# Optimization experiments

Hardware: AMD Instinct MI355X
Metric: run time of the kernel (lower is better)

Reference implementation:

```python
import jax, jax.numpy as jnp
import numpy as np
from jax import lax

H = 128  # hidden_size
E = 4    # embed_size
L = 4    # num_layers


def gru_cell(x, h, wih, whh, bih, bhh):
    # x: [B, in], h: [B, H]; PyTorch gate order: r, z, n
    gi = x @ wih.T + bih          # [B, 3H]
    gh = h @ whh.T + bhh          # [B, 3H]
    ir, iz, inn = jnp.split(gi, 3, axis=-1)
    hr, hz, hn = jnp.split(gh, 3, axis=-1)
    r = jax.nn.sigmoid(ir + hr)
    z = jax.nn.sigmoid(iz + hz)
    n = jnp.tanh(inn + r * hn)
    return (1.0 - z) * n + z * h


def multilayer_gru_step(hidden, x_t, wih0, whh0, wih, whh, bih, bhh):
    # hidden: [L, B, H], x_t: [B, E] -> (new_hidden [L,B,H], top_out [B,H])
    hs = []
    h0 = gru_cell(x_t, hidden[0], wih0, whh0, bih[0], bhh[0])
    hs.append(h0)
    inp = h0
    for l in range(1, L):
        hl = gru_cell(inp, hidden[l], wih[l - 1], whh[l - 1], bih[l], bhh[l])
        hs.append(hl)
        inp = hl
    return jnp.stack(hs, axis=0), inp


def setup_inputs() -> dict:
    key = jax.random.key(0)
    ks = jax.random.split(key, 20)
    s = 1.0 / np.sqrt(H)
    u = lambda k, shp: jax.random.uniform(k, shp, jnp.float32, -s, s)
    inp = {
        'inp_tensor': jax.random.normal(ks[0], (4096, 64, E), jnp.float32),
        'tgt_tensor': jax.random.normal(ks[1], (4096, 100, E), jnp.float32),
        # encoder GRU params
        'enc_wih0': u(ks[2], (3 * H, E)),
        'enc_whh0': u(ks[3], (3 * H, H)),
        'enc_wih': u(ks[4], (L - 1, 3 * H, H)),
        'enc_whh': u(ks[5], (L - 1, 3 * H, H)),
        'enc_bih': u(ks[6], (L, 3 * H)),
        'enc_bhh': u(ks[7], (L, 3 * H)),
        # decoder GRU params
        'dec_wih0': u(ks[8], (3 * H, E)),
        'dec_whh0': u(ks[9], (3 * H, H)),
        'dec_wih': u(ks[10], (L - 1, 3 * H, H)),
        'dec_whh': u(ks[11], (L - 1, 3 * H, H)),
        'dec_bih': u(ks[12], (L, 3 * H)),
        'dec_bhh': u(ks[13], (L, 3 * H)),
        # decoder MLP params
        'lin1_w': u(ks[14], (H, H)),
        'lin1_b': u(ks[15], (H,)),
        'lin2_w': u(ks[16], (E, H)),
        'lin2_b': u(ks[17], (E,)),
    }
    return inp


def reference(inp_tensor, tgt_tensor, enc_wih0, enc_whh0, enc_wih, enc_whh,
              enc_bih, enc_bhh, dec_wih0, dec_whh0, dec_wih, dec_whh,
              dec_bih, dec_bhh, lin1_w, lin1_b, lin2_w, lin2_b):
    B = inp_tensor.shape[0]
    T = tgt_tensor.shape[1]

    # ---- encoder: scan over source time ----
    h_init = jnp.zeros((L, B, H), inp_tensor.dtype)

    def enc_step(hidden, x_t):
        new_h, top = multilayer_gru_step(hidden, x_t, enc_wih0, enc_whh0,
                                         enc_wih, enc_whh, enc_bih, enc_bhh)
        return new_h, top

    enc_hidden, enc_outs = lax.scan(enc_step, h_init,
                                    jnp.transpose(inp_tensor, (1, 0, 2)))
    encoder_output = jnp.transpose(enc_outs, (1, 0, 2))  # [B, S, H]

    # ---- decoder: teacher forcing, target_length-1 steps ----
    # decoder inputs: [inp[:,0], tgt[:,1], ..., tgt[:,T-2]]; tgt part detached
    dec_inputs = jnp.concatenate(
        [inp_tensor[:, 0:1, :], lax.stop_gradient(tgt_tensor[:, 1:T - 1, :])], axis=1)
    dec_targets = tgt_tensor[:, 1:T, :]  # [B, T-1, E]

    def dec_step(hidden, xy):
        x_t, y_t = xy
        new_h, top = multilayer_gru_step(hidden, x_t, dec_wih0, dec_whh0,
                                         dec_wih, dec_whh, dec_bih, dec_bhh)
        o = jax.nn.relu(top @ lin1_w.T + lin1_b) @ lin2_w.T + lin2_b  # [B, E]
        step_loss = jnp.mean((o - y_t) ** 2)
        return new_h, (o, step_loss)

    dec_hidden, (dec_outs, step_losses) = lax.scan(
        dec_step, enc_hidden,
        (jnp.transpose(dec_inputs, (1, 0, 2)), jnp.transpose(dec_targets, (1, 0, 2))))
    loss = jnp.sum(step_losses)
    decoder_output = jnp.concatenate(
        [inp_tensor[:, 0:1, :], jnp.transpose(dec_outs, (1, 0, 2))], axis=1)  # [B, T, E]

    return decoder_output, dec_hidden, encoder_output, enc_hidden, loss
```

## Files before the change

kernel.cpp:

```cpp
#include <hip/hip_runtime.h>

#define T_ENC 64
#define T_DEC 99

#define SLOT    16384
#define PH_BLOB 393216
#define O_LIN1  786432
#define W_TOTAL 802816

#define DEC_OUT_OFF 0
#define DEC_HID_OFF 1638400
#define ENC_OUT_OFF 3735552
#define ENC_HID_OFF 37289984
#define LOSS_OFF    39387136

typedef float f32x4 __attribute__((ext_vector_type(4)));
typedef int   v8i  __attribute__((ext_vector_type(8)));
typedef long  v4l  __attribute__((ext_vector_type(4)));

__device__ __forceinline__ v8i as8i(v4l x) {
  union { v4l l; v8i i; } u; u.l = x; return u.i;
}

__device__ __forceinline__ void keep(v4l &x) { asm volatile("" : "+v"(x)); }
__device__ __forceinline__ void keep(long &x) { asm volatile("" : "+v"(x)); }

#define MFMA8(a, b, c) __builtin_amdgcn_mfma_f32_16x16x32_fp8_fp8((a), (b), (c), 0, 0, 0)
#define MFMAS(a, b, c) \
  __builtin_amdgcn_mfma_scale_f32_16x16x128_f8f6f4(as8i(a), as8i(b), (c), 0, 0, 0, 127, 0, 127)

__device__ __forceinline__ unsigned f2fp8pk(float a, float b) {
  return (unsigned)__builtin_amdgcn_cvt_pk_fp8_f32(a, b, 0, false);
}
__device__ __forceinline__ float sigm(float x) {
  return __builtin_amdgcn_rcpf(1.f + __expf(-x));
}
__device__ __forceinline__ float tanh_fast(float x) {
  x = fminf(fmaxf(x, -15.f), 15.f);
  float e = __expf(-2.f * x);
  return (1.f - e) * __builtin_amdgcn_rcpf(1.f + e);
}

__global__ void convert_weights(const float* __restrict__ ewih0, const float* __restrict__ ewhh0,
                                const float* __restrict__ ewih, const float* __restrict__ ewhh,
                                const float* __restrict__ dwih0, const float* __restrict__ dwhh0,
                                const float* __restrict__ dwih, const float* __restrict__ dwhh,
                                const float* __restrict__ lin1w, unsigned char* __restrict__ wb) {
  int i = blockIdx.x * 256 + threadIdx.x;
  if (i >= W_TOTAL) return;
  float v;
  if (i < O_LIN1) {
    const int ph = i / PH_BLOB;
    const int li = i % PH_BLOB;
    const float* wih0 = ph ? dwih0 : ewih0;
    const float* whh0 = ph ? dwhh0 : ewhh0;
    const float* wih  = ph ? dwih  : ewih;
    const float* whh  = ph ? dwhh  : ewhh;
    const int l = li / (6 * SLOT);
    const int r6 = li % (6 * SLOT);
    const int s = r6 / SLOT, r = r6 % SLOT;
    const int g = (s < 3) ? s : (s - 3);
    if (s >= 3 && l == 0) {
      const int w = r >> 11, ks = (r >> 9) & 3, lane = (r >> 3) & 63, e = r & 7;
      const int quad = lane >> 4, ln = lane & 15;
      const int row = g * 128 + w * 16 + ln;
      const int col = ks * 32 + quad * 8 + e;
      v = (col < 4) ? wih0[row * 4 + col] : 0.f;
    } else {
      const int w = r >> 11, lane = (r >> 5) & 63, b = r & 31;
      const int quad = lane >> 4, ln = lane & 15;
      const int row = g * 128 + w * 16 + ln;
      const int col = quad * 32 + b;
      v = (s < 3) ? ((l == 0) ? whh0[row * 128 + col]
                              : whh[(l - 1) * 49152 + row * 128 + col])
                  : wih[(l - 1) * 49152 + row * 128 + col];
    }
  } else {
    const int r = i - O_LIN1;
    const int w = r >> 11, lane = (r >> 5) & 63, b = r & 31;
    const int quad = lane >> 4, ln = lane & 15;
    v = lin1w[(w * 16 + ln) * 128 + quad * 32 + b];
  }
  wb[i] = (unsigned char)(f2fp8pk(v, v) & 0xFF);
}

__global__ void zero_loss_k(float* out) { out[LOSS_OFF] = 0.f; }

__global__ __launch_bounds__(512, 2) void gru_seq2seq(
    const float* __restrict__ inp, const float* __restrict__ tgt,
    const float* __restrict__ enc_bih, const float* __restrict__ enc_bhh,
    const float* __restrict__ dec_bih, const float* __restrict__ dec_bhh,
    const float* __restrict__ lin1_b, const float* __restrict__ lin2_w,
    const float* __restrict__ lin2_b, const unsigned char* __restrict__ wb,
    float* __restrict__ out) {
  const int tid = threadIdx.x;
  const int wave = tid >> 6;
  const int lane = tid & 63;
  const int ln = lane & 15;
  const int quad = lane >> 4;
  const int b0 = blockIdx.x * 16;
  const int j = (wave << 4) + ln;

  __shared__ __align__(16) unsigned char hb8[2][4][16][128];
  __shared__ __align__(16) unsigned char xt8[2][16][128];
  __shared__ float bsum[4][2][128];
  __shared__ float bnn[4][2][128];
  __shared__ float lin1bs[128];
  __shared__ __align__(16) float lin2ws[4][132];
  __shared__ float lin2bs[4];
  __shared__ __align__(16) float relu_s[16][132];

  for (int i = tid; i < 2 * 4 * 16 * 128; i += 512) ((unsigned char*)hb8)[i] = 0;
  for (int i = tid; i < 2 * 16 * 128; i += 512) ((unsigned char*)xt8)[i] = 0;
  if (tid < 128) lin1bs[tid] = lin1_b[tid];
  { int e = tid >> 7, k = tid & 127; lin2ws[e][k] = lin2_w[e * 128 + k]; }
  if (tid < 4) lin2bs[tid] = lin2_b[tid];

  float hreg[4][4];
#pragma unroll
  for (int l = 0; l < 4; l++)
#pragma unroll
    for (int r = 0; r < 4; r++) hreg[l][r] = 0.f;

  float loss_local = 0.f;

  if (tid < 64) {
    int m = tid >> 2, e = tid & 3;
    out[DEC_OUT_OFF + (b0 + m) * 400 + e] = inp[(b0 + m) * 256 + e];
  }

  const int fofs32 = wave * 2048 + lane * 32;
  const int fofs8  = wave * 2048 + lane * 8;

  v4l w1v = *(const v4l*)(wb + O_LIN1 + fofs32);
  keep(w1v);

#pragma unroll 1
  for (int ph = 0; ph < 2; ph++) {
    const float* bih = ph ? dec_bih : enc_bih;
    const float* bhh = ph ? dec_bhh : enc_bhh;
    {
      int l = tid >> 7, jj = tid & 127;
      bsum[l][0][jj] = bih[l * 384 + jj] + bhh[l * 384 + jj];
      bsum[l][1][jj] = bih[l * 384 + 128 + jj] + bhh[l * 384 + 128 + jj];
      bnn[l][0][jj] = bih[l * 384 + 256 + jj];
      bnn[l][1][jj] = bhh[l * 384 + 256 + jj];
    }
    if (tid < 64) {
      int m = tid >> 2, e = tid & 3;
      xt8[0][m][(m << 3) | e] =
          (unsigned char)(f2fp8pk(inp[(b0 + m) * 256 + e], 0.f) & 0xFF);
    }
    __syncthreads();

    const unsigned char* PB = wb + ph * PH_BLOB;
    v4l whv[4][3];
    v4l wxv[3][3];
    long wx0f[3];
#pragma unroll
    for (int l = 0; l < 4; l++)
#pragma unroll
      for (int g = 0; g < 3; g++) {
        whv[l][g] = *(const v4l*)(PB + l * 6 * SLOT + g * SLOT + fofs32);
        keep(whv[l][g]);
      }
#pragma unroll
    for (int l = 1; l < 4; l++)
#pragma unroll
      for (int g = 0; g < 3; g++) {
        wxv[l - 1][g] = *(const v4l*)(PB + l * 6 * SLOT + (3 + g) * SLOT + fofs32);
        keep(wxv[l - 1][g]);
      }
#pragma unroll
    for (int g = 0; g < 3; g++) {
      wx0f[g] = *(const long*)(PB + (3 + g) * SLOT + fofs8);
      keep(wx0f[g]);
    }

    const float l1b = lin1bs[j];
    const int T = ph ? T_DEC : T_ENC;

#pragma unroll 1
    for (int t = 0; t < T; t++) {
      const int p = t & 1;
#pragma unroll
      for (int l = 0; l < 4; l++) {
        f32x4 ar = {0.f, 0.f, 0.f, 0.f}, az = {0.f, 0.f, 0.f, 0.f};
        f32x4 ani = {0.f, 0.f, 0.f, 0.f}, anh = {0.f, 0.f, 0.f, 0.f};
        {
          const unsigned char* ahb = &hb8[1 - p][l][0][0] + ln * 128;
          v4l Ah;
#pragma unroll
          for (int i4 = 0; i4 < 4; i4++)
            Ah[i4] = *(const long*)(ahb + ((((quad * 4 + i4) ^ ln) << 3)));
          ar  = MFMAS(Ah, whv[l][0], ar);
          az  = MFMAS(Ah, whv[l][1], az);
          anh = MFMAS(Ah, whv[l][2], anh);
        }
        if (l > 0) {
          const unsigned char* axb = &hb8[p][l - 1][0][0] + ln * 128;
          v4l Ax;
#pragma unroll
          for (int i4 = 0; i4 < 4; i4++)
            Ax[i4] = *(const long*)(axb + ((((quad * 4 + i4) ^ ln) << 3)));
          ar  = MFMAS(Ax, wxv[l - 1][0], ar);
          az  = MFMAS(Ax, wxv[l - 1][1], az);
          ani = MFMAS(Ax, wxv[l - 1][2], ani);
        } else {
          const unsigned char* axb = &xt8[p][0][0] + ln * 128;
          const long a_x0 = *(const long*)(axb + ((quad ^ ln) << 3));
          ar  = MFMA8(a_x0, wx0f[0], ar);
          az  = MFMA8(a_x0, wx0f[1], az);
          ani = MFMA8(a_x0, wx0f[2], ani);
        }
        const float brl = bsum[l][0][j], bzl = bsum[l][1][j];
        const float binl = bnn[l][0][j], bhnl = bnn[l][1][j];
        float hnv[4];
#pragma unroll
        for (int r = 0; r < 4; r++) {
          const int m = quad * 4 + r;
          const float hp = hreg[l][r];
          const float rg = sigm(ar[r] + brl);
          const float zg = sigm(az[r] + bzl);
          const float ng = tanh_fast(ani[r] + binl + rg * (anh[r] + bhnl));
          const float hn = (1.f - zg) * ng + zg * hp;
          hreg[l][r] = hn;
          hnv[r] = hn;
          if (!ph) {
            if (l == 3) out[ENC_OUT_OFF + ((b0 + m) * 64 + t) * 128 + j] = hn;
            if (t == T_ENC - 1) out[ENC_HID_OFF + (l * 4096 + b0 + m) * 128 + j] = hn;
          } else if (t == T_DEC - 1) {
            out[DEC_HID_OFF + (l * 4096 + b0 + m) * 128 + j] = hn;
          }
        }
        {
          unsigned pkA = f2fp8pk(hnv[0], hnv[1]);
          unsigned pkB = f2fp8pk(hnv[2], hnv[3]);
          unsigned char* hw = &hb8[p][l][0][0];
          const int m0 = quad * 4;
#pragma unroll
          for (int r = 0; r < 4; r++) {
            const int m = m0 + r;
            const unsigned pk = (r < 2) ? pkA : pkB;
            hw[m * 128 + ((((j >> 3) ^ m) << 3) | (j & 7))] =
                (unsigned char)((pk >> ((r & 1) * 8)) & 0xFF);
          }
        }
        if (l == 3 && (t + 1) < T && tid < 64) {
          int m = tid >> 2, e = tid & 3;
          float xv = ph ? tgt[(b0 + m) * 400 + (t + 1) * 4 + e]
                        : inp[(b0 + m) * 256 + (t + 1) * 4 + e];
          xt8[1 - p][m][(m << 3) | e] = (unsigned char)(f2fp8pk(xv, 0.f) & 0xFF);
        }
        __syncthreads();
      }

      if (ph) {
        f32x4 a1 = {0.f, 0.f, 0.f, 0.f};
        {
          const unsigned char* h3 = &hb8[p][3][0][0] + ln * 128;
          v4l Ah3;
#pragma unroll
          for (int i4 = 0; i4 < 4; i4++)
            Ah3[i4] = *(const long*)(h3 + ((((quad * 4 + i4) ^ ln) << 3)));
          a1 = MFMAS(Ah3, w1v, a1);
        }
#pragma unroll
        for (int r = 0; r < 4; r++) {
          const int m = quad * 4 + r;
          const float v = a1[r] + l1b;
          relu_s[m][j] = v > 0.f ? v : 0.f;
        }
        __syncthreads();
        {
          const int m2 = tid >> 5, e2 = (tid >> 3) & 3, kg = tid & 7;
          const float4* rs = (const float4*)&relu_s[m2][kg * 16];
          const float4* ws = (const float4*)&lin2ws[e2][kg * 16];
          float a0 = 0.f, a1p = 0.f;
#pragma unroll
          for (int q = 0; q < 4; q += 2) {
            float4 r0 = rs[q], w0 = ws[q];
            float4 r1 = rs[q + 1], w1 = ws[q + 1];
            a0 += r0.x * w0.x + r0.y * w0.y + r0.z * w0.z + r0.w * w0.w;
            a1p += r1.x * w1.x + r1.y * w1.y + r1.z * w1.z + r1.w * w1.w;
          }
          float acc = a0 + a1p;
          acc += __shfl_down(acc, 4);
          acc += __shfl_down(acc, 2);
          acc += __shfl_down(acc, 1);
          if (kg == 0) {
            acc += lin2bs[e2];
            const int oidx = (b0 + m2) * 400 + (t + 1) * 4 + e2;
            out[DEC_OUT_OFF + oidx] = acc;
            const float d = acc - tgt[oidx];
            loss_local += d * d;
          }
        }
      }
    }
  }

  loss_local *= (1.f / 16384.f);
#pragma unroll
  for (int off = 32; off; off >>= 1) loss_local += __shfl_down(loss_local, off);
  if (lane == 0) atomicAdd(&out[LOSS_OFF], loss_local);
}

extern "C" void kernel_launch(void* const* d_in, const int* in_sizes, int n_in,
                              void* d_out, int out_size, void* d_ws, size_t ws_size,
                              hipStream_t stream) {
  const float* inp      = (const float*)d_in[0];
  const float* tgt      = (const float*)d_in[1];
  const float* enc_wih0 = (const float*)d_in[2];
  const float* enc_whh0 = (const float*)d_in[3];
  const float* enc_wih  = (const float*)d_in[4];
  const float* enc_whh  = (const float*)d_in[5];
  const float* enc_bih  = (const float*)d_in[6];
  const float* enc_bhh  = (const float*)d_in[7];
  const float* dec_wih0 = (const float*)d_in[8];
  const float* dec_whh0 = (const float*)d_in[9];
  const float* dec_wih  = (const float*)d_in[10];
  const float* dec_whh  = (const float*)d_in[11];
  const float* dec_bih  = (const float*)d_in[12];
  const float* dec_bhh  = (const float*)d_in[13];
  const float* lin1_w   = (const float*)d_in[14];
  const float* lin1_b   = (const float*)d_in[15];
  const float* lin2_w   = (const float*)d_in[16];
  const float* lin2_b   = (const float*)d_in[17];
  unsigned char* wb = (unsigned char*)d_ws;
  float* out = (float*)d_out;

  hipLaunchKernelGGL(convert_weights, dim3((W_TOTAL + 255) / 256), dim3(256), 0, stream,
                     enc_wih0, enc_whh0, enc_wih, enc_whh, dec_wih0, dec_whh0, dec_wih,
                     dec_whh, lin1_w, wb);
  hipLaunchKernelGGL(zero_loss_k, dim3(1), dim3(1), 0, stream, out);
  hipLaunchKernelGGL(gru_seq2seq, dim3(256), dim3(512), 0, stream,
                     inp, tgt, enc_bih, enc_bhh, dec_bih, dec_bhh,
                     lin1_b, lin2_w, lin2_b, wb, out);
}
```

Before: 927.0 us.

## Wavefront-pipeline GRU layers and MLP head across timesteps with one barrier per diagonal

Restructures the time loop into a diagonal wavefront: at step d, layer l processes timestep d-l, and the decoder MLP's two stages are skewed by one and two further steps. The four layers and the MLP stages no longer depend on each other within a step, so the per-layer __syncthreads calls and the extra MLP barrier collapse into a single barrier per diagonal. Invalid edge steps write to a trash buffer and keep the old hidden state. Output stores are moved after the layer loop and read from registers. The cost is five extra pipeline fill and drain iterations, wasted MFMA work at the edges, and a double-buffered relu buffer.

```diff
diff --git a/kernel.cpp b/kernel.cpp
--- a/kernel.cpp
+++ b/kernel.cpp
@@ -103,12 +103,13 @@
 
   __shared__ __align__(16) unsigned char hb8[2][4][16][128];
   __shared__ __align__(16) unsigned char xt8[2][16][128];
+  __shared__ __align__(16) unsigned char trash[2048];
   __shared__ float bsum[4][2][128];
   __shared__ float bnn[4][2][128];
   __shared__ float lin1bs[128];
   __shared__ __align__(16) float lin2ws[4][132];
   __shared__ float lin2bs[4];
-  __shared__ __align__(16) float relu_s[16][132];
+  __shared__ __align__(16) float relu_s[2][16][132];
 
   for (int i = tid; i < 2 * 4 * 16 * 128; i += 512) ((unsigned char*)hb8)[i] = 0;
   for (int i = tid; i < 2 * 16 * 128; i += 512) ((unsigned char*)xt8)[i] = 0;
@@ -179,12 +180,16 @@
 
     const float l1b = lin1bs[j];
     const int T = ph ? T_DEC : T_ENC;
+    const int Dtot = ph ? (T_DEC + 5) : (T_ENC + 3);
 
 #pragma unroll 1
-    for (int t = 0; t < T; t++) {
-      const int p = t & 1;
+    for (int d = 0; d < Dtot; d++) {
+      const int p = d & 1;
+
 #pragma unroll
       for (int l = 0; l < 4; l++) {
+        const int t = d - l;
+        const bool valid = (t >= 0) && (t < T);
         f32x4 ar = {0.f, 0.f, 0.f, 0.f}, az = {0.f, 0.f, 0.f, 0.f};
         f32x4 ani = {0.f, 0.f, 0.f, 0.f}, anh = {0.f, 0.f, 0.f, 0.f};
         {
@@ -198,7 +203,7 @@
           anh = MFMAS(Ah, whv[l][2], anh);
         }
         if (l > 0) {
-          const unsigned char* axb = &hb8[p][l - 1][0][0] + ln * 128;
+          const unsigned char* axb = &hb8[1 - p][l - 1][0][0] + ln * 128;
           v4l Ax;
 #pragma unroll
           for (int i4 = 0; i4 < 4; i4++)
@@ -218,25 +223,18 @@
         float hnv[4];
 #pragma unroll
         for (int r = 0; r < 4; r++) {
-          const int m = quad * 4 + r;
           const float hp = hreg[l][r];
           const float rg = sigm(ar[r] + brl);
           const float zg = sigm(az[r] + bzl);
           const float ng = tanh_fast(ani[r] + binl + rg * (anh[r] + bhnl));
           const float hn = (1.f - zg) * ng + zg * hp;
-          hreg[l][r] = hn;
+          hreg[l][r] = valid ? hn : hp;
           hnv[r] = hn;
-          if (!ph) {
-            if (l == 3) out[ENC_OUT_OFF + ((b0 + m) * 64 + t) * 128 + j] = hn;
-            if (t == T_ENC - 1) out[ENC_HID_OFF + (l * 4096 + b0 + m) * 128 + j] = hn;
-          } else if (t == T_DEC - 1) {
-            out[DEC_HID_OFF + (l * 4096 + b0 + m) * 128 + j] = hn;
-          }
         }
         {
           unsigned pkA = f2fp8pk(hnv[0], hnv[1]);
           unsigned pkB = f2fp8pk(hnv[2], hnv[3]);
-          unsigned char* hw = &hb8[p][l][0][0];
+          unsigned char* hw = valid ? &hb8[p][l][0][0] : &trash[0];
           const int m0 = quad * 4;
 #pragma unroll
           for (int r = 0; r < 4; r++) {
@@ -246,35 +244,66 @@
                 (unsigned char)((pk >> ((r & 1) * 8)) & 0xFF);
           }
         }
-        if (l == 3 && (t + 1) < T && tid < 64) {
-          int m = tid >> 2, e = tid & 3;
-          float xv = ph ? tgt[(b0 + m) * 400 + (t + 1) * 4 + e]
-                        : inp[(b0 + m) * 256 + (t + 1) * 4 + e];
-          xt8[1 - p][m][(m << 3) | e] = (unsigned char)(f2fp8pk(xv, 0.f) & 0xFF);
-        }
-        __syncthreads();
+      }
+
+      if (!ph) {
+        const int t3 = d - 3;
+        if (t3 >= 0) {
+#pragma unroll
+          for (int r = 0; r < 4; r++) {
+            const int m = quad * 4 + r;
+            out[ENC_OUT_OFF + ((b0 + m) * 64 + t3) * 128 + j] = hreg[3][r];
+          }
+        }
+#pragma unroll
+        for (int ll = 0; ll < 4; ll++)
+          if (d == T_ENC - 1 + ll) {
+#pragma unroll
+            for (int r = 0; r < 4; r++) {
+              const int m = quad * 4 + r;
+              out[ENC_HID_OFF + (ll * 4096 + b0 + m) * 128 + j] = hreg[ll][r];
+            }
+          }
+      } else {
+#pragma unroll
+        for (int ll = 0; ll < 4; ll++)
+          if (d == T_DEC - 1 + ll) {
+#pragma unroll
+            for (int r = 0; r < 4; r++) {
+              const int m = quad * 4 + r;
+              out[DEC_HID_OFF + (ll * 4096 + b0 + m) * 128 + j] = hreg[ll][r];
+            }
+          }
+      }
+
+      if ((d + 1) < T && tid < 64) {
+        int m = tid >> 2, e = tid & 3;
+        float xv = ph ? tgt[(b0 + m) * 400 + (d + 1) * 4 + e]
+                      : inp[(b0 + m) * 256 + (d + 1) * 4 + e];
+        xt8[1 - p][m][(m << 3) | e] = (unsigned char)(f2fp8pk(xv, 0.f) & 0xFF);
       }
 
       if (ph) {
-        f32x4 a1 = {0.f, 0.f, 0.f, 0.f};
-        {
-          const unsigned char* h3 = &hb8[p][3][0][0] + ln * 128;
+        const int t1 = d - 4;
+        if (t1 >= 0 && t1 < T_DEC) {
+          f32x4 a1 = {0.f, 0.f, 0.f, 0.f};
+          const unsigned char* h3 = &hb8[1 - p][3][0][0] + ln * 128;
           v4l Ah3;
 #pragma unroll
           for (int i4 = 0; i4 < 4; i4++)
             Ah3[i4] = *(const long*)(h3 + ((((quad * 4 + i4) ^ ln) << 3)));
           a1 = MFMAS(Ah3, w1v, a1);
-        }
-#pragma unroll
-        for (int r = 0; r < 4; r++) {
-          const int m = quad * 4 + r;
-          const float v = a1[r] + l1b;
-          relu_s[m][j] = v > 0.f ? v : 0.f;
-        }
-        __syncthreads();
-        {
+#pragma unroll
+          for (int r = 0; r < 4; r++) {
+            const int m = quad * 4 + r;
+            const float v = a1[r] + l1b;
+            relu_s[p][m][j] = v > 0.f ? v : 0.f;
+          }
+        }
+        const int t2 = d - 5;
+        if (t2 >= 0) {
           const int m2 = tid >> 5, e2 = (tid >> 3) & 3, kg = tid & 7;
-          const float4* rs = (const float4*)&relu_s[m2][kg * 16];
+          const float4* rs = (const float4*)&relu_s[1 - p][m2][kg * 16];
           const float4* ws = (const float4*)&lin2ws[e2][kg * 16];
           float a0 = 0.f, a1p = 0.f;
 #pragma unroll
@@ -290,13 +319,15 @@
           acc += __shfl_down(acc, 1);
           if (kg == 0) {
             acc += lin2bs[e2];
-            const int oidx = (b0 + m2) * 400 + (t + 1) * 4 + e2;
+            const int oidx = (b0 + m2) * 400 + (t2 + 1) * 4 + e2;
             out[DEC_OUT_OFF + oidx] = acc;
-            const float d = acc - tgt[oidx];
-            loss_local += d * d;
-          }
-        }
-      }
+            const float d2 = acc - tgt[oidx];
+            loss_local += d2 * d2;
+          }
+        }
+      }
+
+      __syncthreads();
     }
   }
 
```

After: 813.6 us. -12.2%, faster.
